# Performance work log

Hardware: AMD Instinct MI355X
Metric: run time of the kernel (lower is better)

The kernel has to match this reference:

```python
import jax, jax.numpy as jnp
import numpy as np

NH = 5   # num_multiheads (forced by the 5 gamma parameters)
FH = 64  # filters_head == in_dim (forced by residual broadcast)


def setup_inputs() -> dict:
    key = jax.random.key(0)
    k1, k2, k3 = jax.random.split(key, 3)
    B, C, D, H, W = 4, FH, 8, 64, 64
    x = jax.random.normal(k1, (B, C, D, H, W), dtype=jnp.float32)
    # pointwise qkv projection (stand-in for RBF_modified2d): in_dim -> 3*NH*FH
    Wqkv = jax.random.normal(k2, (3 * NH * FH, C), dtype=jnp.float32) * 0.02
    bqkv = jnp.zeros((3 * NH * FH,), dtype=jnp.float32)
    # gammas init to zeros in torch; use random values so attention path contributes
    gamma = jax.random.uniform(k3, (NH,), dtype=jnp.float32)
    return {"x": x, "Wqkv": Wqkv, "bqkv": bqkv, "gamma": gamma}


def reference(x, Wqkv, bqkv, gamma):
    B, C, D, H, W = x.shape
    # pointwise projection: (B, 3*NH*FH, D, H, W)
    qkv = jnp.einsum('bcdhw,oc->bodhw', x, Wqkv) + bqkv[None, :, None, None, None]
    # 'b (nh c) d h w -> b nh c d h w' with c = 3*FH, then chunk into q,k,v
    qkv = qkv.reshape(B, NH, 3 * FH, D, H, W)
    q, k, v = qkv[:, :, :FH], qkv[:, :, FH:2 * FH], qkv[:, :, 2 * FH:]
    # sim = k @ q^T over the last two (spatial) dims: (b,nh,c,d,H,H)
    sim = jnp.einsum('bncdiw,bncdjw->bncdij', k, q)
    att = jax.nn.softmax(sim, axis=-1)
    # att @ v -> (b, nh, c, d, H, W)
    pv = jnp.einsum('bncdij,bncdjw->bncdiw', att, v)
    # rearrange 'b nh c d h w -> b (c nh) d h w'
    out_att = pv.transpose(0, 2, 1, 3, 4, 5).reshape(B, FH * NH, D, H, W)
    # chunk into NH heads along merged channel axis -> (B, NH, FH, D, H, W)
    heads = out_att.reshape(B, NH, FH, D, H, W)
    # stack([gamma_i * head_i + x for i]) -> (NH, B, C, D, H, W)
    result = gamma[None, :, None, None, None, None] * heads + x[:, None]
    # rearrange 'nh b c d h w -> b (c nh) d h w'
    result = result.transpose(0, 2, 1, 3, 4, 5)  # (B, C, NH, D, H, W)
    return result.reshape(B, C * NH, D, H, W)
```

## Files before the change

### kernel.cpp

```cpp
#include <hip/hip_runtime.h>
#include <hip/hip_bf16.h>

typedef __bf16 bf16x8 __attribute__((ext_vector_type(8)));
typedef float  f32x4  __attribute__((ext_vector_type(4)));

#define NHEAD 5

__global__ __launch_bounds__(256) void k0_xpose(const float* __restrict__ x,
                                                __bf16* __restrict__ xbf,
                                                int slice_base) {
  int blk = blockIdx.x;
  int ls = blk >> 4;
  int pt = blk & 15;
  int g  = slice_base + ls;
  int b = g >> 3, d = g & 7;
  __shared__ __attribute__((aligned(16))) float xs[64][257];
  const int t = threadIdx.x;
  const int wv = t >> 6, l = t & 63;
  const float* xbase = x + (((size_t)b * 64) * 8 + d) * 4096 + pt * 256;
  for (int i = 0; i < 16; ++i) {
    int row = i * 4 + wv;
    int col = l * 4;
    float4 v = *(const float4*)(xbase + (size_t)row * 32768 + col);
    xs[row][col + 0] = v.x; xs[row][col + 1] = v.y;
    xs[row][col + 2] = v.z; xs[row][col + 3] = v.w;
  }
  __syncthreads();
  for (int i = 0; i < 8; ++i) {
    int chunk = i * 256 + t;
    int p = chunk >> 3, cb = chunk & 7;
    bf16x8 o;
    for (int j = 0; j < 8; ++j) o[j] = (__bf16)xs[cb * 8 + j][p];
    *(bf16x8*)(xbf + ((size_t)ls * 4096 + pt * 256 + p) * 64 + cb * 8) = o;
  }
}

__global__ __launch_bounds__(256) void k1_qkv(const __bf16* __restrict__ xbf,
                                              const float* __restrict__ W,
                                              const float* __restrict__ bias,
                                              __bf16* __restrict__ qkv,
                                              int slice_base) {
  int blk = blockIdx.x;
  int ls = blk / 240;
  int r  = blk % 240;
  int ot = r >> 4;
  int pt = r & 15;
  int o0 = ot * 64;
  __shared__ __attribute__((aligned(16))) __bf16 wlds[64 * 72];
  __shared__ float blds[64];
  __shared__ __attribute__((aligned(16))) __bf16 xt[256 * 72];
  const int t = threadIdx.x;
  for (int i = 0; i < 4; ++i) {
    int e = i * 1024 + t * 4;
    int row = e >> 6, col = e & 63;
    float4 v = *(const float4*)(W + (size_t)o0 * 64 + e);
    __bf16* dst = wlds + row * 72 + col;
    dst[0] = (__bf16)v.x; dst[1] = (__bf16)v.y; dst[2] = (__bf16)v.z; dst[3] = (__bf16)v.w;
  }
  if (t < 64) blds[t] = bias[o0 + t];
  const __bf16* xsrc = xbf + (size_t)ls * 262144 + (size_t)pt * 16384;
  for (int i = 0; i < 8; ++i) {
    int e = (i * 256 + t) * 8;
    int p = e >> 6, c0 = e & 63;
    *(bf16x8*)(xt + p * 72 + c0) = *(const bf16x8*)(xsrc + e);
  }
  __syncthreads();
  const int wv = t >> 6, l = t & 63;
  const int lr = l & 15, g4 = l >> 4;
  const f32x4 zero4 = {0.f, 0.f, 0.f, 0.f};
  bf16x8 a0 = *(const bf16x8*)(wlds + (16 * wv + lr) * 72 + g4 * 8);
  bf16x8 a1 = *(const bf16x8*)(wlds + (16 * wv + lr) * 72 + 32 + g4 * 8);
  f32x4 acc[16];
  for (int i = 0; i < 16; ++i) acc[i] = zero4;
  for (int p2 = 0; p2 < 16; ++p2) {
    const __bf16* xrow = xt + (p2 * 16 + lr) * 72 + g4 * 8;
    bf16x8 b0 = *(const bf16x8*)(xrow);
    bf16x8 b1 = *(const bf16x8*)(xrow + 32);
    acc[p2] = __builtin_amdgcn_mfma_f32_16x16x32_bf16(a0, b0, acc[p2], 0, 0, 0);
    acc[p2] = __builtin_amdgcn_mfma_f32_16x16x32_bf16(a1, b1, acc[p2], 0, 0, 0);
  }
  float bv[4];
  for (int rr = 0; rr < 4; ++rr) bv[rr] = blds[16 * wv + 4 * g4 + rr];
  __syncthreads();
  __bf16* rp = xt;
  for (int p2 = 0; p2 < 16; ++p2)
    for (int rr = 0; rr < 4; ++rr) {
      int o_l = 16 * wv + 4 * g4 + rr;
      rp[o_l * 264 + p2 * 16 + lr] = (__bf16)(acc[p2][rr] + bv[rr]);
    }
  __syncthreads();
  for (int i = 0; i < 8; ++i) {
    int chunk = i * 256 + t;
    int row = chunk >> 5, cb = chunk & 31;
    bf16x8 v = *(const bf16x8*)(rp + row * 264 + cb * 8);
    *(bf16x8*)(qkv + ((size_t)ls * 960 + o0 + row) * 4096 + (size_t)pt * 256 + cb * 8) = v;
  }
}

__global__ __launch_bounds__(256, 3) void k2_attn(const __bf16* __restrict__ qkv,
                                                  const float* __restrict__ x,
                                                  const float* __restrict__ gamma,
                                                  float* __restrict__ out,
                                                  int slice_base) {
  __shared__ __attribute__((aligned(16))) __bf16 buf[2][3][4096];
  int nb = blockIdx.x;
  int ls = nb / 80;
  int r  = nb % 80;
  int n  = r >> 4;
  int cg = r & 15;
  int g = slice_base + ls;
  int b = g >> 3, d = g & 7;

  const int t = threadIdx.x;
  const int wv = t >> 6, l = t & 63, lr = l & 15, g4 = l >> 4;
  const int i0 = wv * 16;
  const int srow = t >> 2;
  const int scol = (t & 3) * 16;
  const f32x4 zero4 = {0.f, 0.f, 0.f, 0.f};

  const __bf16* base = qkv + (size_t)(ls * 960 + n * 192 + cg * 4) * 4096;

  bf16x8 rq0, rq1, rk0, rk1, rv0, rv1;
  f32x4 xpre[4];

#define LOADA(A)                                                        \
  {                                                                     \
    const __bf16* qp = base + (size_t)(A) * 4096;                       \
    const __bf16* kp = qp + (size_t)64 * 4096;                          \
    const __bf16* vp = qp + (size_t)128 * 4096;                         \
    rq0 = *(const bf16x8*)(qp + srow * 64 + scol);                      \
    rq1 = *(const bf16x8*)(qp + srow * 64 + scol + 8);                  \
    rk0 = *(const bf16x8*)(kp + srow * 64 + scol);                      \
    rk1 = *(const bf16x8*)(kp + srow * 64 + scol + 8);                  \
    rv0 = *(const bf16x8*)(vp + srow * 64 + scol);                      \
    rv1 = *(const bf16x8*)(vp + srow * 64 + scol + 8);                  \
  }

#define STOREA(CUR)                                                     \
  {                                                                     \
    int a0 = (srow * 64 + scol) ^ ((srow & 7) << 3);                    \
    int a1 = (srow * 64 + scol + 8) ^ ((srow & 7) << 3);                \
    *(bf16x8*)(&buf[CUR][0][a0]) = rq0;                                 \
    *(bf16x8*)(&buf[CUR][0][a1]) = rq1;                                 \
    *(bf16x8*)(&buf[CUR][1][a0]) = rk0;                                 \
    *(bf16x8*)(&buf[CUR][1][a1]) = rk1;                                 \
    for (int kk = 0; kk < 8; ++kk) {                                    \
      int w0 = scol + kk, w1 = scol + 8 + kk;                           \
      buf[CUR][2][(w0 * 64 + srow) ^ ((w0 & 7) << 3)] = rv0[kk];        \
      buf[CUR][2][(w1 * 64 + srow) ^ ((w1 & 7) << 3)] = rv1[kk];        \
    }                                                                   \
  }

#define PREFX(A)                                                        \
  {                                                                     \
    int o2 = (cg * 4 + (A)) * NHEAD + n;                                \
    int fp = o2 & 63;                                                   \
    const float* xp = x + (((size_t)b * 64 + fp) * 8 + d) * 4096 + t * 16; \
    xpre[0] = *(const f32x4*)(xp);                                      \
    xpre[1] = *(const f32x4*)(xp + 4);                                  \
    xpre[2] = *(const f32x4*)(xp + 8);                                  \
    xpre[3] = *(const f32x4*)(xp + 12);                                 \
  }

  LOADA(0)
  STOREA(0)
  PREFX(0)
  __syncthreads();

  for (int a = 0; a < 4; ++a) {
    const int cur = a & 1;
    if (a < 3) LOADA(a + 1)

    f32x4 sacc[4];
#pragma unroll
    for (int jt = 0; jt < 4; ++jt) sacc[jt] = zero4;
    bf16x8 ka0, ka1;
    {
      int ia = i0 + lr;
      ka0 = *(const bf16x8*)(&buf[cur][1][(ia * 64 + g4 * 8) ^ ((ia & 7) << 3)]);
      ka1 = *(const bf16x8*)(&buf[cur][1][(ia * 64 + 32 + g4 * 8) ^ ((ia & 7) << 3)]);
    }
#pragma unroll
    for (int jt = 0; jt < 4; ++jt) {
      int ja = jt * 16 + lr;
      bf16x8 qb0 = *(const bf16x8*)(&buf[cur][0][(ja * 64 + g4 * 8) ^ ((ja & 7) << 3)]);
      bf16x8 qb1 = *(const bf16x8*)(&buf[cur][0][(ja * 64 + 32 + g4 * 8) ^ ((ja & 7) << 3)]);
      sacc[jt] = __builtin_amdgcn_mfma_f32_16x16x32_bf16(ka0, qb0, sacc[jt], 0, 0, 0);
      sacc[jt] = __builtin_amdgcn_mfma_f32_16x16x32_bf16(ka1, qb1, sacc[jt], 0, 0, 0);
    }

    float pr[4][4];
#pragma unroll
    for (int rr = 0; rr < 4; ++rr) {
      float m = fmaxf(fmaxf(sacc[0][rr], sacc[1][rr]), fmaxf(sacc[2][rr], sacc[3][rr]));
#pragma unroll
      for (int dd = 1; dd < 16; dd <<= 1) m = fmaxf(m, __shfl_xor(m, dd));
      float s = 0.f;
#pragma unroll
      for (int jt = 0; jt < 4; ++jt) {
        pr[jt][rr] = __expf(sacc[jt][rr] - m);
        s += pr[jt][rr];
      }
#pragma unroll
      for (int dd = 1; dd < 16; dd <<= 1) s += __shfl_xor(s, dd);
      float inv = 1.0f / s;
#pragma unroll
      for (int jt = 0; jt < 4; ++jt) pr[jt][rr] *= inv;
    }
    __syncthreads();

#pragma unroll
    for (int jt = 0; jt < 4; ++jt)
#pragma unroll
      for (int rr = 0; rr < 4; ++rr) {
        int i = i0 + 4 * g4 + rr;
        int j = jt * 16 + lr;
        buf[cur][1][(i * 64 + j) ^ ((i & 7) << 3)] = (__bf16)pr[jt][rr];
      }
    __syncthreads();

    f32x4 pacc[4];
#pragma unroll
    for (int wt = 0; wt < 4; ++wt) pacc[wt] = zero4;
    bf16x8 aa0, aa1;
    {
      int ia = i0 + lr;
      aa0 = *(const bf16x8*)(&buf[cur][1][(ia * 64 + g4 * 8) ^ ((ia & 7) << 3)]);
      aa1 = *(const bf16x8*)(&buf[cur][1][(ia * 64 + 32 + g4 * 8) ^ ((ia & 7) << 3)]);
    }
#pragma unroll
    for (int wt = 0; wt < 4; ++wt) {
      int wrow = wt * 16 + lr;
      bf16x8 vb0 = *(const bf16x8*)(&buf[cur][2][(wrow * 64 + g4 * 8) ^ ((wrow & 7) << 3)]);
      bf16x8 vb1 = *(const bf16x8*)(&buf[cur][2][(wrow * 64 + 32 + g4 * 8) ^ ((wrow & 7) << 3)]);
      pacc[wt] = __builtin_amdgcn_mfma_f32_16x16x32_bf16(aa0, vb0, pacc[wt], 0, 0, 0);
      pacc[wt] = __builtin_amdgcn_mfma_f32_16x16x32_bf16(aa1, vb1, pacc[wt], 0, 0, 0);
    }
    __syncthreads();

    if (a < 3) STOREA(cur ^ 1)

    float* fb = (float*)&buf[cur][0][0];
#pragma unroll
    for (int wt = 0; wt < 4; ++wt)
#pragma unroll
      for (int rr = 0; rr < 4; ++rr) {
        int i = i0 + 4 * g4 + rr;
        int w = wt * 16 + lr;
        fb[(i * 64 + w) ^ ((i & 7) << 2)] = pacc[wt][rr];
      }
    __syncthreads();

    {
      int o2 = (cg * 4 + a) * NHEAD + n;
      int np = o2 >> 6, fp = o2 & 63;
      int oc = fp * NHEAD + np;
      float gm = gamma[np];
      int ib = t >> 2;
      int xs_ = ((ib & 7) << 2);
      f32x4 p0 = *(const f32x4*)(fb + ((t * 16 + 0) ^ xs_));
      f32x4 p1 = *(const f32x4*)(fb + ((t * 16 + 4) ^ xs_));
      f32x4 p2 = *(const f32x4*)(fb + ((t * 16 + 8) ^ xs_));
      f32x4 p3 = *(const f32x4*)(fb + ((t * 16 + 12) ^ xs_));
      f32x4 o0, o1, o2v, o3;
#pragma unroll
      for (int j = 0; j < 4; ++j) {
        o0[j] = gm * p0[j] + xpre[0][j];
        o1[j] = gm * p1[j] + xpre[1][j];
        o2v[j] = gm * p2[j] + xpre[2][j];
        o3[j] = gm * p3[j] + xpre[3][j];
      }
      float* op = out + (((size_t)b * 320 + oc) * 8 + d) * 4096 + t * 16;
      *(f32x4*)(op + 0) = o0;
      *(f32x4*)(op + 4) = o1;
      *(f32x4*)(op + 8) = o2v;
      *(f32x4*)(op + 12) = o3;
    }
    if (a < 3) PREFX(a + 1)
  }
#undef LOADA
#undef STOREA
#undef PREFX
}

extern "C" void kernel_launch(void* const* d_in, const int* in_sizes, int n_in,
                              void* d_out, int out_size, void* d_ws, size_t ws_size,
                              hipStream_t stream) {
  const float* x     = (const float*)d_in[0];
  const float* W     = (const float*)d_in[1];
  const float* bias  = (const float*)d_in[2];
  const float* gamma = (const float*)d_in[3];
  float* out = (float*)d_out;

  const size_t per_slice = 524288 + 7864320;
  int S = (int)(ws_size / per_slice);
  if (S > 32) S = 32;
  if (S < 1)  S = 1;
  __bf16* xbf = (__bf16*)d_ws;
  __bf16* qkv = (__bf16*)((char*)d_ws + (size_t)S * 524288);

  for (int sb = 0; sb < 32; sb += S) {
    int sc = 32 - sb; if (sc > S) sc = S;
    k0_xpose<<<16  * sc, 256, 0, stream>>>(x, xbf, sb);
    k1_qkv  <<<240 * sc, 256, 0, stream>>>(xbf, W, bias, qkv, sb);
    k2_attn <<<80  * sc, 256, 0, stream>>>(qkv, x, gamma, out, sb);
  }
}
```

Measured before the change: 196.8 us.

## Process one channel per attention block and cap slices per launch round

```diff
diff --git a/kernel.cpp b/kernel.cpp
--- a/kernel.cpp
+++ b/kernel.cpp
@@ -97,17 +97,17 @@
   }
 }
 
-__global__ __launch_bounds__(256, 3) void k2_attn(const __bf16* __restrict__ qkv,
+__global__ __launch_bounds__(256, 5) void k2_attn(const __bf16* __restrict__ qkv,
                                                   const float* __restrict__ x,
                                                   const float* __restrict__ gamma,
                                                   float* __restrict__ out,
                                                   int slice_base) {
-  __shared__ __attribute__((aligned(16))) __bf16 buf[2][3][4096];
+  __shared__ __attribute__((aligned(16))) __bf16 buf[3][4096];
   int nb = blockIdx.x;
-  int ls = nb / 80;
-  int r  = nb % 80;
-  int n  = r >> 4;
-  int cg = r & 15;
+  int ls = nb / 320;
+  int r  = nb % 320;
+  int n  = r >> 6;
+  int c  = r & 63;
   int g = slice_base + ls;
   int b = g >> 3, d = g & 7;
 
@@ -118,169 +118,144 @@
   const int scol = (t & 3) * 16;
   const f32x4 zero4 = {0.f, 0.f, 0.f, 0.f};
 
-  const __bf16* base = qkv + (size_t)(ls * 960 + n * 192 + cg * 4) * 4096;
-
-  bf16x8 rq0, rq1, rk0, rk1, rv0, rv1;
+  const __bf16* qp = qkv + (size_t)(ls * 960 + n * 192 + c) * 4096;
+  const __bf16* kp = qp + (size_t)64 * 4096;
+  const __bf16* vp = qp + (size_t)128 * 4096;
+
+  {
+    bf16x8 rq0 = *(const bf16x8*)(qp + srow * 64 + scol);
+    bf16x8 rq1 = *(const bf16x8*)(qp + srow * 64 + scol + 8);
+    bf16x8 rk0 = *(const bf16x8*)(kp + srow * 64 + scol);
+    bf16x8 rk1 = *(const bf16x8*)(kp + srow * 64 + scol + 8);
+    bf16x8 rv0 = *(const bf16x8*)(vp + srow * 64 + scol);
+    bf16x8 rv1 = *(const bf16x8*)(vp + srow * 64 + scol + 8);
+    int a0 = (srow * 64 + scol) ^ ((srow & 7) << 3);
+    int a1 = (srow * 64 + scol + 8) ^ ((srow & 7) << 3);
+    *(bf16x8*)(&buf[0][a0]) = rq0;
+    *(bf16x8*)(&buf[0][a1]) = rq1;
+    *(bf16x8*)(&buf[1][a0]) = rk0;
+    *(bf16x8*)(&buf[1][a1]) = rk1;
+#pragma unroll
+    for (int kk = 0; kk < 8; ++kk) {
+      int w0 = scol + kk, w1 = scol + 8 + kk;
+      buf[2][(w0 * 64 + srow) ^ ((w0 & 7) << 3)] = rv0[kk];
+      buf[2][(w1 * 64 + srow) ^ ((w1 & 7) << 3)] = rv1[kk];
+    }
+  }
+
   f32x4 xpre[4];
-
-#define LOADA(A)                                                        \
-  {                                                                     \
-    const __bf16* qp = base + (size_t)(A) * 4096;                       \
-    const __bf16* kp = qp + (size_t)64 * 4096;                          \
-    const __bf16* vp = qp + (size_t)128 * 4096;                         \
-    rq0 = *(const bf16x8*)(qp + srow * 64 + scol);                      \
-    rq1 = *(const bf16x8*)(qp + srow * 64 + scol + 8);                  \
-    rk0 = *(const bf16x8*)(kp + srow * 64 + scol);                      \
-    rk1 = *(const bf16x8*)(kp + srow * 64 + scol + 8);                  \
-    rv0 = *(const bf16x8*)(vp + srow * 64 + scol);                      \
-    rv1 = *(const bf16x8*)(vp + srow * 64 + scol + 8);                  \
-  }
-
-#define STOREA(CUR)                                                     \
-  {                                                                     \
-    int a0 = (srow * 64 + scol) ^ ((srow & 7) << 3);                    \
-    int a1 = (srow * 64 + scol + 8) ^ ((srow & 7) << 3);                \
-    *(bf16x8*)(&buf[CUR][0][a0]) = rq0;                                 \
-    *(bf16x8*)(&buf[CUR][0][a1]) = rq1;                                 \
-    *(bf16x8*)(&buf[CUR][1][a0]) = rk0;                                 \
-    *(bf16x8*)(&buf[CUR][1][a1]) = rk1;                                 \
-    for (int kk = 0; kk < 8; ++kk) {                                    \
-      int w0 = scol + kk, w1 = scol + 8 + kk;                           \
-      buf[CUR][2][(w0 * 64 + srow) ^ ((w0 & 7) << 3)] = rv0[kk];        \
-      buf[CUR][2][(w1 * 64 + srow) ^ ((w1 & 7) << 3)] = rv1[kk];        \
-    }                                                                   \
-  }
-
-#define PREFX(A)                                                        \
-  {                                                                     \
-    int o2 = (cg * 4 + (A)) * NHEAD + n;                                \
-    int fp = o2 & 63;                                                   \
-    const float* xp = x + (((size_t)b * 64 + fp) * 8 + d) * 4096 + t * 16; \
-    xpre[0] = *(const f32x4*)(xp);                                      \
-    xpre[1] = *(const f32x4*)(xp + 4);                                  \
-    xpre[2] = *(const f32x4*)(xp + 8);                                  \
-    xpre[3] = *(const f32x4*)(xp + 12);                                 \
-  }
-
-  LOADA(0)
-  STOREA(0)
-  PREFX(0)
-  __syncthreads();
-
-  for (int a = 0; a < 4; ++a) {
-    const int cur = a & 1;
-    if (a < 3) LOADA(a + 1)
-
-    f32x4 sacc[4];
-#pragma unroll
-    for (int jt = 0; jt < 4; ++jt) sacc[jt] = zero4;
-    bf16x8 ka0, ka1;
-    {
-      int ia = i0 + lr;
-      ka0 = *(const bf16x8*)(&buf[cur][1][(ia * 64 + g4 * 8) ^ ((ia & 7) << 3)]);
-      ka1 = *(const bf16x8*)(&buf[cur][1][(ia * 64 + 32 + g4 * 8) ^ ((ia & 7) << 3)]);
-    }
+  int o2 = c * NHEAD + n;
+  int np = o2 >> 6, fp = o2 & 63;
+  {
+    const float* xp = x + (((size_t)b * 64 + fp) * 8 + d) * 4096 + t * 16;
+    xpre[0] = *(const f32x4*)(xp);
+    xpre[1] = *(const f32x4*)(xp + 4);
+    xpre[2] = *(const f32x4*)(xp + 8);
+    xpre[3] = *(const f32x4*)(xp + 12);
+  }
+  __syncthreads();
+
+  f32x4 sacc[4];
+#pragma unroll
+  for (int jt = 0; jt < 4; ++jt) sacc[jt] = zero4;
+  bf16x8 ka0, ka1;
+  {
+    int ia = i0 + lr;
+    ka0 = *(const bf16x8*)(&buf[1][(ia * 64 + g4 * 8) ^ ((ia & 7) << 3)]);
+    ka1 = *(const bf16x8*)(&buf[1][(ia * 64 + 32 + g4 * 8) ^ ((ia & 7) << 3)]);
+  }
+#pragma unroll
+  for (int jt = 0; jt < 4; ++jt) {
+    int ja = jt * 16 + lr;
+    bf16x8 qb0 = *(const bf16x8*)(&buf[0][(ja * 64 + g4 * 8) ^ ((ja & 7) << 3)]);
+    bf16x8 qb1 = *(const bf16x8*)(&buf[0][(ja * 64 + 32 + g4 * 8) ^ ((ja & 7) << 3)]);
+    sacc[jt] = __builtin_amdgcn_mfma_f32_16x16x32_bf16(ka0, qb0, sacc[jt], 0, 0, 0);
+    sacc[jt] = __builtin_amdgcn_mfma_f32_16x16x32_bf16(ka1, qb1, sacc[jt], 0, 0, 0);
+  }
+
+  float pr[4][4];
+#pragma unroll
+  for (int rr = 0; rr < 4; ++rr) {
+    float m = fmaxf(fmaxf(sacc[0][rr], sacc[1][rr]), fmaxf(sacc[2][rr], sacc[3][rr]));
+#pragma unroll
+    for (int dd = 1; dd < 16; dd <<= 1) m = fmaxf(m, __shfl_xor(m, dd));
+    float s = 0.f;
 #pragma unroll
     for (int jt = 0; jt < 4; ++jt) {
-      int ja = jt * 16 + lr;
-      bf16x8 qb0 = *(const bf16x8*)(&buf[cur][0][(ja * 64 + g4 * 8) ^ ((ja & 7) << 3)]);
-      bf16x8 qb1 = *(const bf16x8*)(&buf[cur][0][(ja * 64 + 32 + g4 * 8) ^ ((ja & 7) << 3)]);
-      sacc[jt] = __builtin_amdgcn_mfma_f32_16x16x32_bf16(ka0, qb0, sacc[jt], 0, 0, 0);
-      sacc[jt] = __builtin_amdgcn_mfma_f32_16x16x32_bf16(ka1, qb1, sacc[jt], 0, 0, 0);
-    }
-
-    float pr[4][4];
+      pr[jt][rr] = __expf(sacc[jt][rr] - m);
+      s += pr[jt][rr];
+    }
+#pragma unroll
+    for (int dd = 1; dd < 16; dd <<= 1) s += __shfl_xor(s, dd);
+    float inv = 1.0f / s;
+#pragma unroll
+    for (int jt = 0; jt < 4; ++jt) pr[jt][rr] *= inv;
+  }
+  __syncthreads();
+
+#pragma unroll
+  for (int jt = 0; jt < 4; ++jt)
 #pragma unroll
     for (int rr = 0; rr < 4; ++rr) {
-      float m = fmaxf(fmaxf(sacc[0][rr], sacc[1][rr]), fmaxf(sacc[2][rr], sacc[3][rr]));
-#pragma unroll
-      for (int dd = 1; dd < 16; dd <<= 1) m = fmaxf(m, __shfl_xor(m, dd));
-      float s = 0.f;
-#pragma unroll
-      for (int jt = 0; jt < 4; ++jt) {
-        pr[jt][rr] = __expf(sacc[jt][rr] - m);
-        s += pr[jt][rr];
-      }
-#pragma unroll
-      for (int dd = 1; dd < 16; dd <<= 1) s += __shfl_xor(s, dd);
-      float inv = 1.0f / s;
-#pragma unroll
-      for (int jt = 0; jt < 4; ++jt) pr[jt][rr] *= inv;
-    }
-    __syncthreads();
-
-#pragma unroll
-    for (int jt = 0; jt < 4; ++jt)
-#pragma unroll
-      for (int rr = 0; rr < 4; ++rr) {
-        int i = i0 + 4 * g4 + rr;
-        int j = jt * 16 + lr;
-        buf[cur][1][(i * 64 + j) ^ ((i & 7) << 3)] = (__bf16)pr[jt][rr];
-      }
-    __syncthreads();
-
-    f32x4 pacc[4];
-#pragma unroll
-    for (int wt = 0; wt < 4; ++wt) pacc[wt] = zero4;
-    bf16x8 aa0, aa1;
-    {
-      int ia = i0 + lr;
-      aa0 = *(const bf16x8*)(&buf[cur][1][(ia * 64 + g4 * 8) ^ ((ia & 7) << 3)]);
-      aa1 = *(const bf16x8*)(&buf[cur][1][(ia * 64 + 32 + g4 * 8) ^ ((ia & 7) << 3)]);
-    }
-#pragma unroll
-    for (int wt = 0; wt < 4; ++wt) {
-      int wrow = wt * 16 + lr;
-      bf16x8 vb0 = *(const bf16x8*)(&buf[cur][2][(wrow * 64 + g4 * 8) ^ ((wrow & 7) << 3)]);
-      bf16x8 vb1 = *(const bf16x8*)(&buf[cur][2][(wrow * 64 + 32 + g4 * 8) ^ ((wrow & 7) << 3)]);
-      pacc[wt] = __builtin_amdgcn_mfma_f32_16x16x32_bf16(aa0, vb0, pacc[wt], 0, 0, 0);
-      pacc[wt] = __builtin_amdgcn_mfma_f32_16x16x32_bf16(aa1, vb1, pacc[wt], 0, 0, 0);
-    }
-    __syncthreads();
-
-    if (a < 3) STOREA(cur ^ 1)
-
-    float* fb = (float*)&buf[cur][0][0];
-#pragma unroll
-    for (int wt = 0; wt < 4; ++wt)
-#pragma unroll
-      for (int rr = 0; rr < 4; ++rr) {
-        int i = i0 + 4 * g4 + rr;
-        int w = wt * 16 + lr;
-        fb[(i * 64 + w) ^ ((i & 7) << 2)] = pacc[wt][rr];
-      }
-    __syncthreads();
-
-    {
-      int o2 = (cg * 4 + a) * NHEAD + n;
-      int np = o2 >> 6, fp = o2 & 63;
-      int oc = fp * NHEAD + np;
-      float gm = gamma[np];
-      int ib = t >> 2;
-      int xs_ = ((ib & 7) << 2);
-      f32x4 p0 = *(const f32x4*)(fb + ((t * 16 + 0) ^ xs_));
-      f32x4 p1 = *(const f32x4*)(fb + ((t * 16 + 4) ^ xs_));
-      f32x4 p2 = *(const f32x4*)(fb + ((t * 16 + 8) ^ xs_));
-      f32x4 p3 = *(const f32x4*)(fb + ((t * 16 + 12) ^ xs_));
-      f32x4 o0, o1, o2v, o3;
-#pragma unroll
-      for (int j = 0; j < 4; ++j) {
-        o0[j] = gm * p0[j] + xpre[0][j];
-        o1[j] = gm * p1[j] + xpre[1][j];
-        o2v[j] = gm * p2[j] + xpre[2][j];
-        o3[j] = gm * p3[j] + xpre[3][j];
-      }
-      float* op = out + (((size_t)b * 320 + oc) * 8 + d) * 4096 + t * 16;
-      *(f32x4*)(op + 0) = o0;
-      *(f32x4*)(op + 4) = o1;
-      *(f32x4*)(op + 8) = o2v;
-      *(f32x4*)(op + 12) = o3;
-    }
-    if (a < 3) PREFX(a + 1)
-  }
-#undef LOADA
-#undef STOREA
-#undef PREFX
+      int i = i0 + 4 * g4 + rr;
+      int j = jt * 16 + lr;
+      buf[1][(i * 64 + j) ^ ((i & 7) << 3)] = (__bf16)pr[jt][rr];
+    }
+  __syncthreads();
+
+  f32x4 pacc[4];
+#pragma unroll
+  for (int wt = 0; wt < 4; ++wt) pacc[wt] = zero4;
+  bf16x8 aa0, aa1;
+  {
+    int ia = i0 + lr;
+    aa0 = *(const bf16x8*)(&buf[1][(ia * 64 + g4 * 8) ^ ((ia & 7) << 3)]);
+    aa1 = *(const bf16x8*)(&buf[1][(ia * 64 + 32 + g4 * 8) ^ ((ia & 7) << 3)]);
+  }
+#pragma unroll
+  for (int wt = 0; wt < 4; ++wt) {
+    int wrow = wt * 16 + lr;
+    bf16x8 vb0 = *(const bf16x8*)(&buf[2][(wrow * 64 + g4 * 8) ^ ((wrow & 7) << 3)]);
+    bf16x8 vb1 = *(const bf16x8*)(&buf[2][(wrow * 64 + 32 + g4 * 8) ^ ((wrow & 7) << 3)]);
+    pacc[wt] = __builtin_amdgcn_mfma_f32_16x16x32_bf16(aa0, vb0, pacc[wt], 0, 0, 0);
+    pacc[wt] = __builtin_amdgcn_mfma_f32_16x16x32_bf16(aa1, vb1, pacc[wt], 0, 0, 0);
+  }
+  __syncthreads();
+
+  float* fb = (float*)&buf[0][0];
+#pragma unroll
+  for (int wt = 0; wt < 4; ++wt)
+#pragma unroll
+    for (int rr = 0; rr < 4; ++rr) {
+      int i = i0 + 4 * g4 + rr;
+      int w = wt * 16 + lr;
+      fb[(i * 64 + w) ^ ((i & 7) << 2)] = pacc[wt][rr];
+    }
+  __syncthreads();
+
+  {
+    int oc = fp * NHEAD + np;
+    float gm = gamma[np];
+    int ib = t >> 2;
+    int xs_ = ((ib & 7) << 2);
+    f32x4 p0 = *(const f32x4*)(fb + ((t * 16 + 0) ^ xs_));
+    f32x4 p1 = *(const f32x4*)(fb + ((t * 16 + 4) ^ xs_));
+    f32x4 p2 = *(const f32x4*)(fb + ((t * 16 + 8) ^ xs_));
+    f32x4 p3 = *(const f32x4*)(fb + ((t * 16 + 12) ^ xs_));
+    f32x4 o0, o1, o2v, o3;
+#pragma unroll
+    for (int j = 0; j < 4; ++j) {
+      o0[j]  = gm * p0[j] + xpre[0][j];
+      o1[j]  = gm * p1[j] + xpre[1][j];
+      o2v[j] = gm * p2[j] + xpre[2][j];
+      o3[j]  = gm * p3[j] + xpre[3][j];
+    }
+    float* op = out + (((size_t)b * 320 + oc) * 8 + d) * 4096 + t * 16;
+    *(f32x4*)(op + 0)  = o0;
+    *(f32x4*)(op + 4)  = o1;
+    *(f32x4*)(op + 8)  = o2v;
+    *(f32x4*)(op + 12) = o3;
+  }
 }
 
 extern "C" void kernel_launch(void* const* d_in, const int* in_sizes, int n_in,
@@ -294,8 +269,8 @@
 
   const size_t per_slice = 524288 + 7864320;
   int S = (int)(ws_size / per_slice);
-  if (S > 32) S = 32;
-  if (S < 1)  S = 1;
+  if (S > 8) S = 8;
+  if (S < 1) S = 1;
   __bf16* xbf = (__bf16*)d_ws;
   __bf16* qkv = (__bf16*)((char*)d_ws + (size_t)S * 524288);
 
@@ -303,6 +278,6 @@
     int sc = 32 - sb; if (sc > S) sc = S;
     k0_xpose<<<16  * sc, 256, 0, stream>>>(x, xbf, sb);
     k1_qkv  <<<240 * sc, 256, 0, stream>>>(xbf, W, bias, qkv, sb);
-    k2_attn <<<80  * sc, 256, 0, stream>>>(qkv, x, gamma, out, sb);
-  }
-}
+    k2_attn <<<320 * sc, 256, 0, stream>>>(qkv, x, gamma, out, sb);
+  }
+}
```

New measurement: 205.8 us. 1.05x slower.
